# Kernel tuning notes

Hardware: AMD Instinct MI355X
Metric: run time of the kernel (lower is better)

The kernel has to match this reference:

```python
import jax, jax.numpy as jnp
import numpy as np

N_NODES = 100000


def _sage_conv(x, src, dst, w_l, b_l, w_r):
    # PyG SAGEConv (aggr='mean', root_weight=True):
    #   out = lin_l(mean_{j in N(i)} x_j) + lin_r(x_i)
    # messages flow src (row 0) -> dst (row 1)
    msgs = x[src]                                             # [E, d]
    agg = jax.ops.segment_sum(msgs, dst, num_segments=N_NODES)  # [N, d]
    cnt = jax.ops.segment_sum(jnp.ones((src.shape[0], 1), x.dtype), dst,
                              num_segments=N_NODES)           # [N, 1]
    mean = agg / jnp.maximum(cnt, 1.0)
    return mean @ w_l + b_l + x @ w_r


def setup_inputs() -> dict:
    key = jax.random.key(0)
    ks = jax.random.split(key, 8)
    in_dim, hid, out = 128, 64, 128
    n_edges = 1600000
    x = jax.random.normal(ks[0], (N_NODES, in_dim), dtype=jnp.float32)
    edge_index = jax.random.randint(ks[1], (2, n_edges), 0, N_NODES, dtype=jnp.int64)
    s1 = 1.0 / np.sqrt(in_dim)
    s2 = 1.0 / np.sqrt(hid)
    return {
        "x": x,
        "edge_index": edge_index,
        "w1_l": jax.random.uniform(ks[2], (in_dim, hid), jnp.float32, -s1, s1),
        "b1": jnp.zeros((hid,), jnp.float32),
        "w1_r": jax.random.uniform(ks[3], (in_dim, hid), jnp.float32, -s1, s1),
        "w2_l": jax.random.uniform(ks[4], (hid, out), jnp.float32, -s2, s2),
        "b2": jnp.zeros((out,), jnp.float32),
        "w2_r": jax.random.uniform(ks[5], (hid, out), jnp.float32, -s2, s2),
    }


def reference(x, edge_index, w1_l, b1, w1_r, w2_l, b2, w2_r):
    src, dst = edge_index[0], edge_index[1]
    h = jax.nn.relu(_sage_conv(x, src, dst, w1_l, b1, w1_r))
    h = _sage_conv(h, src, dst, w2_l, b2, w2_r)
    return h
```

## Files before the change

kernel.cpp:

```cpp
#include <hip/hip_runtime.h>

#define N_NODES 100000
#define NBUCK   782
#define P1TILE  4096
#define SLAB    4096

typedef __bf16 bf16x8 __attribute__((ext_vector_type(8)));
typedef float floatx4 __attribute__((ext_vector_type(4)));
typedef float floatx2 __attribute__((ext_vector_type(2)));

static __device__ __forceinline__ unsigned short f2bf(float f) {
  unsigned u = __float_as_uint(f);
  u += 0x7fff + ((u >> 16) & 1);
  return (unsigned short)(u >> 16);
}

__global__ __launch_bounds__(512) void bucket_partition_kernel(
    const int* __restrict__ src, const int* __restrict__ dst,
    int* __restrict__ bucket_cursor, unsigned* __restrict__ pairs,
    int n_edges, int nb_part,
    const float* __restrict__ w1_l, const float* __restrict__ w1_r,
    const float* __restrict__ w2_l, const float* __restrict__ w2_r,
    unsigned short* __restrict__ Wt1, unsigned short* __restrict__ Wt2) {
  __shared__ int hist[NBUCK];
  __shared__ int scan_[NBUCK];
  __shared__ int gbase[NBUCK];
  __shared__ int tmp[512];
  __shared__ int2 sorted[P1TILE];
  int t = threadIdx.x;

  if ((int)blockIdx.x >= nb_part) {
    int b2 = (int)blockIdx.x - nb_part;
    int n = (b2 << 2) | (t >> 7);
    int k = t & 127;
    float v1 = (n < 64) ? w1_l[k * 64 + n] : w1_r[k * 64 + (n - 64)];
    Wt1[n * 128 + k] = f2bf(v1);
    float v2 = (k < 64) ? w2_l[k * 128 + n] : w2_r[(k - 64) * 128 + n];
    Wt2[n * 128 + k] = f2bf(v2);
    return;
  }

  long e0 = (long)blockIdx.x * P1TILE;
  int n = (int)min((long)P1TILE, (long)n_edges - e0);

  for (int b = t; b < NBUCK; b += 512) hist[b] = 0;
  __syncthreads();
  for (int i = t; i < n; i += 512) atomicAdd(&hist[dst[e0 + i] >> 7], 1);
  __syncthreads();

  int loc[2];
  int s = 0;
  #pragma unroll
  for (int j = 0; j < 2; ++j) {
    int idx = 2 * t + j;
    loc[j] = s;
    s += (idx < NBUCK) ? hist[idx] : 0;
  }
  tmp[t] = s;
  __syncthreads();
  for (int off = 1; off < 512; off <<= 1) {
    int u = (t >= off) ? tmp[t - off] : 0;
    __syncthreads();
    tmp[t] += u;
    __syncthreads();
  }
  int excl = tmp[t] - s;
  #pragma unroll
  for (int j = 0; j < 2; ++j) {
    int idx = 2 * t + j;
    if (idx < NBUCK) scan_[idx] = excl + loc[j];
  }
  __syncthreads();

  for (int b = t; b < NBUCK; b += 512) {
    int c = hist[b];
    gbase[b] = c ? atomicAdd(&bucket_cursor[b], c) : 0;
    hist[b] = scan_[b];
  }
  __syncthreads();

  for (int i = t; i < n; i += 512) {
    int sv = src[e0 + i];
    int dv = dst[e0 + i];
    int r = atomicAdd(&hist[dv >> 7], 1);
    sorted[r] = make_int2(sv, dv);
  }
  __syncthreads();

  for (int i = t; i < n; i += 512) {
    int2 p = sorted[i];
    int b = p.y >> 7;
    int pos = gbase[b] + (i - scan_[b]);
    if (pos < SLAB) {
      unsigned pk = (unsigned)p.x | ((unsigned)(p.y & 127) << 17);
      pairs[(long)b * SLAB + pos] = pk;
    }
  }
}

__global__ __launch_bounds__(512) void bucket_csr_kernel(
    const unsigned* __restrict__ pairs, const int* __restrict__ bucket_cnt,
    int2* __restrict__ offsets2, int* __restrict__ src_sorted, int n_nodes) {
  __shared__ unsigned sp[SLAB];
  __shared__ int lout[SLAB];
  __shared__ int ndeg[128];
  __shared__ int nsc[128];
  int b = blockIdx.x;
  int node0 = b << 7;
  int t = threadIdx.x;
  long sbeg = (long)b * SLAB;
  int m = min(bucket_cnt[b], SLAB);
  if (t < 128) ndeg[t] = 0;
  __syncthreads();

  for (int i = t; i < m; i += 512) {
    unsigned p = pairs[sbeg + i];
    sp[i] = p;
    atomicAdd(&ndeg[p >> 17], 1);
  }
  __syncthreads();

  if (t < 128) nsc[t] = ndeg[t];
  __syncthreads();
  for (int off = 1; off < 128; off <<= 1) {
    int u = 0;
    if (t < 128 && t >= off) u = nsc[t - off];
    __syncthreads();
    if (t < 128) nsc[t] += u;
    __syncthreads();
  }
  if (t < 128) {
    int excl = nsc[t] - ndeg[t];
    int node = node0 + t;
    if (node < n_nodes)
      offsets2[node] = make_int2((int)sbeg + excl, (int)sbeg + nsc[t]);
    ndeg[t] = excl;
  }
  __syncthreads();

  for (int i = t; i < m; i += 512) {
    unsigned p = sp[i];
    int r = atomicAdd(&ndeg[p >> 17], 1);
    lout[r] = (int)(p & 0x1FFFFu);
  }
  __syncthreads();
  for (int i = t; i < m; i += 512) src_sorted[sbeg + i] = lout[i];
}

template <int BIAS_MODE, bool OUT_BF16, bool A_F32>
__global__ __launch_bounds__(256) void mfma_gemm_kernel(
    const void* __restrict__ Av, const unsigned short* __restrict__ Wt,
    const float* __restrict__ bias, void* __restrict__ Y, int M) {
  __shared__ unsigned short As[64 * 136];
  int node0 = blockIdx.x * 64;
  int t = threadIdx.x;
  if (A_F32) {
    const float* A = (const float*)Av;
    #pragma unroll
    for (int i = 0; i < 8; ++i) {
      int c = t + i * 256;
      int row = c >> 5, c4 = (c & 31) * 4;
      float4 v = make_float4(0.f, 0.f, 0.f, 0.f);
      if (node0 + row < M) v = *(const float4*)&A[(long)(node0 + row) * 128 + c4];
      ushort4 o;
      o.x = f2bf(v.x); o.y = f2bf(v.y); o.z = f2bf(v.z); o.w = f2bf(v.w);
      *(ushort4*)&As[row * 136 + c4] = o;
    }
  } else {
    const unsigned short* A = (const unsigned short*)Av;
    #pragma unroll
    for (int i = 0; i < 4; ++i) {
      int c = t + i * 256;
      int row = c >> 4, c8 = (c & 15) * 8;
      uint4 v = make_uint4(0u, 0u, 0u, 0u);
      if (node0 + row < M) v = *(const uint4*)&A[(long)(node0 + row) * 128 + c8];
      *(uint4*)&As[row * 136 + c8] = v;
    }
  }
  __syncthreads();
  int w = t >> 6, lane = t & 63;
  int m = lane & 15, q = lane >> 4;
  int col0 = w * 32;
  floatx4 acc[4][2];
  #pragma unroll
  for (int rt = 0; rt < 4; ++rt)
    #pragma unroll
    for (int ct = 0; ct < 2; ++ct) acc[rt][ct] = (floatx4){0.f, 0.f, 0.f, 0.f};

  #pragma unroll
  for (int ks = 0; ks < 4; ++ks) {
    bf16x8 b0 = *(const bf16x8*)&Wt[(col0 + m) * 128 + ks * 32 + q * 8];
    bf16x8 b1 = *(const bf16x8*)&Wt[(col0 + 16 + m) * 128 + ks * 32 + q * 8];
    #pragma unroll
    for (int rt = 0; rt < 4; ++rt) {
      bf16x8 a = *(const bf16x8*)&As[(rt * 16 + m) * 136 + ks * 32 + q * 8];
      acc[rt][0] = __builtin_amdgcn_mfma_f32_16x16x32_bf16(a, b0, acc[rt][0], 0, 0, 0);
      acc[rt][1] = __builtin_amdgcn_mfma_f32_16x16x32_bf16(a, b1, acc[rt][1], 0, 0, 0);
    }
  }
  #pragma unroll
  for (int ct = 0; ct < 2; ++ct) {
    int col = col0 + ct * 16 + m;
    float bv = 0.f;
    if (BIAS_MODE == 1) bv = (col >= 64) ? bias[col - 64] : 0.f;
    if (BIAS_MODE == 2) bv = bias[col];
    #pragma unroll
    for (int rt = 0; rt < 4; ++rt) {
      #pragma unroll
      for (int i = 0; i < 4; ++i) {
        int row = node0 + rt * 16 + q * 4 + i;
        if (row >= M) continue;
        float v = acc[rt][ct][i] + bv;
        if (OUT_BF16) ((unsigned short*)Y)[(long)row * 128 + col] = f2bf(v);
        else          ((float*)Y)[(long)row * 128 + col] = v;
      }
    }
  }
}

#define ACC_P(A, v)                                                            \
  do {                                                                         \
    A[0] += (floatx2){__uint_as_float((v).x << 16),                            \
                      __uint_as_float((v).x & 0xffff0000u)};                   \
    A[1] += (floatx2){__uint_as_float((v).y << 16),                            \
                      __uint_as_float((v).y & 0xffff0000u)};                   \
    A[2] += (floatx2){__uint_as_float((v).z << 16),                            \
                      __uint_as_float((v).z & 0xffff0000u)};                   \
    A[3] += (floatx2){__uint_as_float((v).w << 16),                            \
                      __uint_as_float((v).w & 0xffff0000u)};                   \
  } while (0)

#define AGG_CAP 512
template <bool FUSE_RELU>
__global__ __launch_bounds__(256) void aggregate_bf16_kernel(
    const unsigned short* __restrict__ gsrc, const unsigned short* __restrict__ zadd,
    unsigned short* __restrict__ outp, const int2* __restrict__ offsets2,
    const int* __restrict__ src_sorted, int n_nodes) {
  __shared__ int stage[4 * AGG_CAP];
  int wv = threadIdx.x >> 6;
  int lane = threadIdx.x & 63;
  int wid = (blockIdx.x << 2) | wv;
  int node8 = wid << 3;
  int sub = lane >> 3;
  int sl  = lane & 7;
  int node = node8 + sub;
  bool wvalid = (node8 < n_nodes);
  bool nvalid = wvalid && (node < n_nodes);

  int wbeg = 0, wend = 0, beg = 0, end = 0;
  if (wvalid) {
    wbeg = offsets2[node8].x;
    wend = offsets2[min(node8 + 8, n_nodes) - 1].y;
  }
  if (nvalid) {
    int2 o = offsets2[node];
    beg = o.x; end = o.y;
  }
  int deg = end - beg;
  int cnt = wend - wbeg;
  int* my = &stage[wv * AGG_CAP];
  bool staged = wvalid && (cnt <= AGG_CAP);
  if (staged) {
    for (int i = lane; i < cnt; i += 64) my[i] = src_sorted[wbeg + i];
  }
  __syncthreads();

  const unsigned short* base = gsrc + sl * 8;
  floatx2 A0[4], A1[4], A2[4], A3[4];
  #pragma unroll
  for (int i = 0; i < 4; ++i) {
    A0[i] = (floatx2){0.f, 0.f}; A1[i] = (floatx2){0.f, 0.f};
    A2[i] = (floatx2){0.f, 0.f}; A3[i] = (floatx2){0.f, 0.f};
  }

  if (staged) {
    int lb = beg - wbeg;
    int e = 0;
    for (; e + 8 <= deg; e += 8) {
      int s0 = my[lb + e];
      int s1 = my[lb + e + 1];
      int s2 = my[lb + e + 2];
      int s3 = my[lb + e + 3];
      int s4 = my[lb + e + 4];
      int s5 = my[lb + e + 5];
      int s6 = my[lb + e + 6];
      int s7 = my[lb + e + 7];
      uint4 v0 = *(const uint4*)(base + (long)s0 * 128);
      uint4 v1 = *(const uint4*)(base + (long)s1 * 128);
      uint4 v2 = *(const uint4*)(base + (long)s2 * 128);
      uint4 v3 = *(const uint4*)(base + (long)s3 * 128);
      uint4 v4 = *(const uint4*)(base + (long)s4 * 128);
      uint4 v5 = *(const uint4*)(base + (long)s5 * 128);
      uint4 v6 = *(const uint4*)(base + (long)s6 * 128);
      uint4 v7 = *(const uint4*)(base + (long)s7 * 128);
      ACC_P(A0, v0); ACC_P(A1, v1); ACC_P(A2, v2); ACC_P(A3, v3);
      ACC_P(A0, v4); ACC_P(A1, v5); ACC_P(A2, v6); ACC_P(A3, v7);
    }
    if (e + 4 <= deg) {
      int s0 = my[lb + e];
      int s1 = my[lb + e + 1];
      int s2 = my[lb + e + 2];
      int s3 = my[lb + e + 3];
      uint4 v0 = *(const uint4*)(base + (long)s0 * 128);
      uint4 v1 = *(const uint4*)(base + (long)s1 * 128);
      uint4 v2 = *(const uint4*)(base + (long)s2 * 128);
      uint4 v3 = *(const uint4*)(base + (long)s3 * 128);
      ACC_P(A0, v0); ACC_P(A1, v1); ACC_P(A2, v2); ACC_P(A3, v3);
      e += 4;
    }
    for (; e < deg; ++e) {
      int s0 = my[lb + e];
      uint4 v0 = *(const uint4*)(base + (long)s0 * 128);
      ACC_P(A0, v0);
    }
  } else if (nvalid) {
    for (int e = beg; e < end; ++e) {
      int s0 = src_sorted[e];
      uint4 v0 = *(const uint4*)(base + (long)s0 * 128);
      ACC_P(A0, v0);
    }
  }
  #pragma unroll
  for (int i = 0; i < 4; ++i) A0[i] = (A0[i] + A1[i]) + (A2[i] + A3[i]);

  if (nvalid) {
    float inv = 1.f / fmaxf((float)deg, 1.f);
    float r[8];
    r[0] = A0[0].x * inv; r[1] = A0[0].y * inv;
    r[2] = A0[1].x * inv; r[3] = A0[1].y * inv;
    r[4] = A0[2].x * inv; r[5] = A0[2].y * inv;
    r[6] = A0[3].x * inv; r[7] = A0[3].y * inv;
    if (FUSE_RELU) {
      uint4 z = *(const uint4*)&zadd[(long)node * 128 + sl * 8];
      r[0] = fmaxf(r[0] + __uint_as_float(z.x << 16), 0.f);
      r[1] = fmaxf(r[1] + __uint_as_float(z.x & 0xffff0000u), 0.f);
      r[2] = fmaxf(r[2] + __uint_as_float(z.y << 16), 0.f);
      r[3] = fmaxf(r[3] + __uint_as_float(z.y & 0xffff0000u), 0.f);
      r[4] = fmaxf(r[4] + __uint_as_float(z.z << 16), 0.f);
      r[5] = fmaxf(r[5] + __uint_as_float(z.z & 0xffff0000u), 0.f);
      r[6] = fmaxf(r[6] + __uint_as_float(z.w << 16), 0.f);
      r[7] = fmaxf(r[7] + __uint_as_float(z.w & 0xffff0000u), 0.f);
    }
    uint4 ov;
    ov.x = (unsigned)f2bf(r[0]) | ((unsigned)f2bf(r[1]) << 16);
    ov.y = (unsigned)f2bf(r[2]) | ((unsigned)f2bf(r[3]) << 16);
    ov.z = (unsigned)f2bf(r[4]) | ((unsigned)f2bf(r[5]) << 16);
    ov.w = (unsigned)f2bf(r[6]) | ((unsigned)f2bf(r[7]) << 16);
    *(uint4*)&outp[(long)node * 128 + sl * 8] = ov;
  }
}
#undef ACC_P

extern "C" void kernel_launch(void* const* d_in, const int* in_sizes, int n_in,
                              void* d_out, int out_size, void* d_ws, size_t ws_size,
                              hipStream_t stream) {
  const float* x    = (const float*)d_in[0];
  const int*   ei   = (const int*)d_in[1];
  const float* w1_l = (const float*)d_in[2];
  const float* b1   = (const float*)d_in[3];
  const float* w1_r = (const float*)d_in[4];
  const float* w2_l = (const float*)d_in[5];
  const float* b2   = (const float*)d_in[6];
  const float* w2_r = (const float*)d_in[7];
  float* out = (float*)d_out;

  const int E = in_sizes[1] / 2;
  const int* src = ei;
  const int* dst = ei + E;

  unsigned short* ZB1 = (unsigned short*)d_ws;
  unsigned*       pairs = (unsigned*)d_ws;
  unsigned short* ZB2 = ZB1 + (long)N_NODES * 128;
  unsigned short* Wt1 = ZB2 + (long)N_NODES * 128;
  unsigned short* Wt2 = Wt1 + 16384;
  int* bucket_cursor = (int*)(Wt2 + 16384);
  int2* offsets2     = (int2*)(bucket_cursor + NBUCK + 2);
  int* src_sorted    = (int*)(offsets2 + N_NODES);

  hipMemsetAsync(bucket_cursor, 0, (size_t)NBUCK * sizeof(int), stream);
  int nb_part = (E + P1TILE - 1) / P1TILE;
  bucket_partition_kernel<<<nb_part + 32, 512, 0, stream>>>(
      src, dst, bucket_cursor, pairs, E, nb_part,
      w1_l, w1_r, w2_l, w2_r, Wt1, Wt2);
  bucket_csr_kernel<<<NBUCK, 512, 0, stream>>>(pairs, bucket_cursor,
                                               offsets2, src_sorted, N_NODES);

  int gemm_blocks = (N_NODES + 63) / 64;
  int agg_blocks = (N_NODES + 31) / 32;

  mfma_gemm_kernel<1, true, true><<<gemm_blocks, 256, 0, stream>>>(
      x, Wt1, b1, ZB1, N_NODES);
  aggregate_bf16_kernel<true><<<agg_blocks, 256, 0, stream>>>(
      ZB1, ZB1 + 64, ZB2 + 64, offsets2, src_sorted, N_NODES);

  aggregate_bf16_kernel<false><<<agg_blocks, 256, 0, stream>>>(
      ZB2 + 64, nullptr, ZB2, offsets2, src_sorted, N_NODES);
  mfma_gemm_kernel<2, false, false><<<gemm_blocks, 256, 0, stream>>>(
      ZB2, Wt2, b2, out, N_NODES);
}
```

Baseline: 244.2 us.

## Fuse layer-1 GEMM into the edge-partition launch and move weight prep to init kernel

Moves the first-layer projection GEMM (x·[W1_l|W1_r]) into the same grid as the edge bucket partition, so the compute-bound GEMM blocks run alongside the atomic-heavy partition blocks instead of in a separate launch. Weight transposition and bucket-cursor zeroing move into a small init kernel that replaces the memset. The pairs buffer gets its own workspace region so it no longer aliases ZB1. The fused kernel uses a shared-memory union and 128-row GEMM tiles on 512 threads, which may lower occupancy for the partition blocks.

```diff
diff --git a/kernel.cpp b/kernel.cpp
--- a/kernel.cpp
+++ b/kernel.cpp
@@ -4,6 +4,7 @@
 #define NBUCK   782
 #define P1TILE  4096
 #define SLAB    4096
+#define AGG_CAP 512
 
 typedef __bf16 bf16x8 __attribute__((ext_vector_type(8)));
 typedef float floatx4 __attribute__((ext_vector_type(4)));
@@ -15,31 +16,85 @@
   return (unsigned short)(u >> 16);
 }
 
-__global__ __launch_bounds__(512) void bucket_partition_kernel(
+__global__ __launch_bounds__(256) void init_kernel(
+    int* __restrict__ bucket_cursor,
+    const float* __restrict__ w1_l, const float* __restrict__ w1_r,
+    const float* __restrict__ w2_l, const float* __restrict__ w2_r,
+    unsigned short* __restrict__ Wt1, unsigned short* __restrict__ Wt2) {
+  int gid = blockIdx.x * 256 + threadIdx.x;
+  if (gid < NBUCK + 2) bucket_cursor[gid] = 0;
+  int n = gid >> 7, k = gid & 127;
+  float v1 = (n < 64) ? w1_l[k * 64 + n] : w1_r[k * 64 + (n - 64)];
+  Wt1[n * 128 + k] = f2bf(v1);
+  float v2 = (k < 64) ? w2_l[k * 128 + n] : w2_r[(k - 64) * 128 + n];
+  Wt2[n * 128 + k] = f2bf(v2);
+}
+
+__global__ __launch_bounds__(512) void part_gemm1_kernel(
     const int* __restrict__ src, const int* __restrict__ dst,
     int* __restrict__ bucket_cursor, unsigned* __restrict__ pairs,
     int n_edges, int nb_part,
-    const float* __restrict__ w1_l, const float* __restrict__ w1_r,
-    const float* __restrict__ w2_l, const float* __restrict__ w2_r,
-    unsigned short* __restrict__ Wt1, unsigned short* __restrict__ Wt2) {
-  __shared__ int hist[NBUCK];
-  __shared__ int scan_[NBUCK];
-  __shared__ int gbase[NBUCK];
-  __shared__ int tmp[512];
-  __shared__ int2 sorted[P1TILE];
+    const float* __restrict__ x, const unsigned short* __restrict__ Wt1,
+    const float* __restrict__ b1, unsigned short* __restrict__ ZB1, int M) {
+  __shared__ __align__(16) char smem[44224];
   int t = threadIdx.x;
 
   if ((int)blockIdx.x >= nb_part) {
-    int b2 = (int)blockIdx.x - nb_part;
-    int n = (b2 << 2) | (t >> 7);
-    int k = t & 127;
-    float v1 = (n < 64) ? w1_l[k * 64 + n] : w1_r[k * 64 + (n - 64)];
-    Wt1[n * 128 + k] = f2bf(v1);
-    float v2 = (k < 64) ? w2_l[k * 128 + n] : w2_r[(k - 64) * 128 + n];
-    Wt2[n * 128 + k] = f2bf(v2);
+    unsigned short* As = (unsigned short*)smem;
+    int node0 = ((int)blockIdx.x - nb_part) * 128;
+    #pragma unroll
+    for (int i = 0; i < 8; ++i) {
+      int c = t + i * 512;
+      int row = c >> 5, c4 = (c & 31) * 4;
+      float4 v = make_float4(0.f, 0.f, 0.f, 0.f);
+      if (node0 + row < M) v = *(const float4*)&x[(long)(node0 + row) * 128 + c4];
+      ushort4 o;
+      o.x = f2bf(v.x); o.y = f2bf(v.y); o.z = f2bf(v.z); o.w = f2bf(v.w);
+      *(ushort4*)&As[row * 136 + c4] = o;
+    }
+    __syncthreads();
+    int w8 = t >> 6, lane = t & 63;
+    int m = lane & 15, q = lane >> 4;
+    int w = w8 & 3, half = w8 >> 2;
+    int col0 = w * 32, rowbase = half * 64;
+    floatx4 acc[4][2];
+    #pragma unroll
+    for (int rt = 0; rt < 4; ++rt)
+      #pragma unroll
+      for (int ct = 0; ct < 2; ++ct) acc[rt][ct] = (floatx4){0.f, 0.f, 0.f, 0.f};
+    #pragma unroll
+    for (int ks = 0; ks < 4; ++ks) {
+      bf16x8 b0 = *(const bf16x8*)&Wt1[(col0 + m) * 128 + ks * 32 + q * 8];
+      bf16x8 bb = *(const bf16x8*)&Wt1[(col0 + 16 + m) * 128 + ks * 32 + q * 8];
+      #pragma unroll
+      for (int rt = 0; rt < 4; ++rt) {
+        bf16x8 a = *(const bf16x8*)&As[(rowbase + rt * 16 + m) * 136 + ks * 32 + q * 8];
+        acc[rt][0] = __builtin_amdgcn_mfma_f32_16x16x32_bf16(a, b0, acc[rt][0], 0, 0, 0);
+        acc[rt][1] = __builtin_amdgcn_mfma_f32_16x16x32_bf16(a, bb, acc[rt][1], 0, 0, 0);
+      }
+    }
+    #pragma unroll
+    for (int ct = 0; ct < 2; ++ct) {
+      int col = col0 + ct * 16 + m;
+      float bv = (col >= 64) ? b1[col - 64] : 0.f;
+      #pragma unroll
+      for (int rt = 0; rt < 4; ++rt) {
+        #pragma unroll
+        for (int i = 0; i < 4; ++i) {
+          int row = node0 + rowbase + rt * 16 + q * 4 + i;
+          if (row >= M) continue;
+          ZB1[(long)row * 128 + col] = f2bf(acc[rt][ct][i] + bv);
+        }
+      }
+    }
     return;
   }
 
+  int2* sorted = (int2*)smem;
+  int* hist  = (int*)(smem + 32768);
+  int* scan_ = hist + NBUCK;
+  int* gbase = scan_ + NBUCK;
+  int* tmp   = gbase + NBUCK;
   long e0 = (long)blockIdx.x * P1TILE;
   int n = (int)min((long)P1TILE, (long)n_edges - e0);
 
@@ -147,35 +202,19 @@
   for (int i = t; i < m; i += 512) src_sorted[sbeg + i] = lout[i];
 }
 
-template <int BIAS_MODE, bool OUT_BF16, bool A_F32>
-__global__ __launch_bounds__(256) void mfma_gemm_kernel(
-    const void* __restrict__ Av, const unsigned short* __restrict__ Wt,
-    const float* __restrict__ bias, void* __restrict__ Y, int M) {
+__global__ __launch_bounds__(256) void mfma_gemm2_kernel(
+    const unsigned short* __restrict__ A, const unsigned short* __restrict__ Wt,
+    const float* __restrict__ bias, float* __restrict__ Y, int M) {
   __shared__ unsigned short As[64 * 136];
   int node0 = blockIdx.x * 64;
   int t = threadIdx.x;
-  if (A_F32) {
-    const float* A = (const float*)Av;
-    #pragma unroll
-    for (int i = 0; i < 8; ++i) {
-      int c = t + i * 256;
-      int row = c >> 5, c4 = (c & 31) * 4;
-      float4 v = make_float4(0.f, 0.f, 0.f, 0.f);
-      if (node0 + row < M) v = *(const float4*)&A[(long)(node0 + row) * 128 + c4];
-      ushort4 o;
-      o.x = f2bf(v.x); o.y = f2bf(v.y); o.z = f2bf(v.z); o.w = f2bf(v.w);
-      *(ushort4*)&As[row * 136 + c4] = o;
-    }
-  } else {
-    const unsigned short* A = (const unsigned short*)Av;
-    #pragma unroll
-    for (int i = 0; i < 4; ++i) {
-      int c = t + i * 256;
-      int row = c >> 4, c8 = (c & 15) * 8;
-      uint4 v = make_uint4(0u, 0u, 0u, 0u);
-      if (node0 + row < M) v = *(const uint4*)&A[(long)(node0 + row) * 128 + c8];
-      *(uint4*)&As[row * 136 + c8] = v;
-    }
+  #pragma unroll
+  for (int i = 0; i < 4; ++i) {
+    int c = t + i * 256;
+    int row = c >> 4, c8 = (c & 15) * 8;
+    uint4 v = make_uint4(0u, 0u, 0u, 0u);
+    if (node0 + row < M) v = *(const uint4*)&A[(long)(node0 + row) * 128 + c8];
+    *(uint4*)&As[row * 136 + c8] = v;
   }
   __syncthreads();
   int w = t >> 6, lane = t & 63;
@@ -201,18 +240,14 @@
   #pragma unroll
   for (int ct = 0; ct < 2; ++ct) {
     int col = col0 + ct * 16 + m;
-    float bv = 0.f;
-    if (BIAS_MODE == 1) bv = (col >= 64) ? bias[col - 64] : 0.f;
-    if (BIAS_MODE == 2) bv = bias[col];
+    float bv = bias[col];
     #pragma unroll
     for (int rt = 0; rt < 4; ++rt) {
       #pragma unroll
       for (int i = 0; i < 4; ++i) {
         int row = node0 + rt * 16 + q * 4 + i;
         if (row >= M) continue;
-        float v = acc[rt][ct][i] + bv;
-        if (OUT_BF16) ((unsigned short*)Y)[(long)row * 128 + col] = f2bf(v);
-        else          ((float*)Y)[(long)row * 128 + col] = v;
+        Y[(long)row * 128 + col] = acc[rt][ct][i] + bv;
       }
     }
   }
@@ -230,7 +265,6 @@
                       __uint_as_float((v).w & 0xffff0000u)};                   \
   } while (0)
 
-#define AGG_CAP 512
 template <bool FUSE_RELU>
 __global__ __launch_bounds__(256) void aggregate_bf16_kernel(
     const unsigned short* __restrict__ gsrc, const unsigned short* __restrict__ zadd,
@@ -369,32 +403,29 @@
   const int* dst = ei + E;
 
   unsigned short* ZB1 = (unsigned short*)d_ws;
-  unsigned*       pairs = (unsigned*)d_ws;
   unsigned short* ZB2 = ZB1 + (long)N_NODES * 128;
   unsigned short* Wt1 = ZB2 + (long)N_NODES * 128;
   unsigned short* Wt2 = Wt1 + 16384;
   int* bucket_cursor = (int*)(Wt2 + 16384);
   int2* offsets2     = (int2*)(bucket_cursor + NBUCK + 2);
   int* src_sorted    = (int*)(offsets2 + N_NODES);
-
-  hipMemsetAsync(bucket_cursor, 0, (size_t)NBUCK * sizeof(int), stream);
+  unsigned* pairs    = (unsigned*)(src_sorted + (long)NBUCK * SLAB);
+
   int nb_part = (E + P1TILE - 1) / P1TILE;
-  bucket_partition_kernel<<<nb_part + 32, 512, 0, stream>>>(
-      src, dst, bucket_cursor, pairs, E, nb_part,
-      w1_l, w1_r, w2_l, w2_r, Wt1, Wt2);
+  int gemm1_blocks = (N_NODES + 127) / 128;
+
+  init_kernel<<<64, 256, 0, stream>>>(bucket_cursor, w1_l, w1_r, w2_l, w2_r,
+                                      Wt1, Wt2);
+  part_gemm1_kernel<<<nb_part + gemm1_blocks, 512, 0, stream>>>(
+      src, dst, bucket_cursor, pairs, E, nb_part, x, Wt1, b1, ZB1, N_NODES);
   bucket_csr_kernel<<<NBUCK, 512, 0, stream>>>(pairs, bucket_cursor,
                                                offsets2, src_sorted, N_NODES);
 
-  int gemm_blocks = (N_NODES + 63) / 64;
   int agg_blocks = (N_NODES + 31) / 32;
-
-  mfma_gemm_kernel<1, true, true><<<gemm_blocks, 256, 0, stream>>>(
-      x, Wt1, b1, ZB1, N_NODES);
   aggregate_bf16_kernel<true><<<agg_blocks, 256, 0, stream>>>(
       ZB1, ZB1 + 64, ZB2 + 64, offsets2, src_sorted, N_NODES);
-
   aggregate_bf16_kernel<false><<<agg_blocks, 256, 0, stream>>>(
       ZB2 + 64, nullptr, ZB2, offsets2, src_sorted, N_NODES);
-  mfma_gemm_kernel<2, false, false><<<gemm_blocks, 256, 0, stream>>>(
+  mfma_gemm2_kernel<<<(N_NODES + 63) / 64, 256, 0, stream>>>(
       ZB2, Wt2, b2, out, N_NODES);
 }
```

After: 237.7 us. 1.03x faster.
